# Kernel tuning notes

Measured on AMD Instinct MI355X. Metric: run time of the kernel, lower is better.

## Reference

```python
import jax, jax.numpy as jnp
import numpy as np

BOX_WARP = 1.0
RAY_START = 2.25
RAY_END = 3.3
S = 32  # depth_resolution (coarse), N_importance = 0


def bilinear_sample(image, coords):
    """Faithful port of the custom grid_sample (align_corners=True mapping).
    image: [B, C, H, W]; coords: [B, M, 2] in [-1, 1]. Returns [B, M, C]."""
    B, C, H, W = image.shape
    ix = (coords[..., 0] + 1.0) * 0.5 * (W - 1)
    iy = (coords[..., 1] + 1.0) * 0.5 * (H - 1)
    ix0 = jnp.floor(ix)
    iy0 = jnp.floor(iy)
    ix1 = ix0 + 1.0
    iy1 = iy0 + 1.0
    # weights use UNclamped corner positions, matching the torch code
    w_nw = (ix1 - ix) * (iy1 - iy)
    w_ne = (ix - ix0) * (iy1 - iy)
    w_sw = (ix1 - ix) * (iy - iy0)
    w_se = (ix - ix0) * (iy - iy0)
    ix0c = jnp.clip(ix0, 0, W - 1).astype(jnp.int32)
    ix1c = jnp.clip(ix1, 0, W - 1).astype(jnp.int32)
    iy0c = jnp.clip(iy0, 0, H - 1).astype(jnp.int32)
    iy1c = jnp.clip(iy1, 0, H - 1).astype(jnp.int32)
    img = image.reshape(B, C, H * W)

    def gather(iyc, ixc):
        idx = iyc * W + ixc  # [B, M]
        return jnp.take_along_axis(img, idx[:, None, :], axis=2)  # [B, C, M]

    out = (gather(iy0c, ix0c) * w_nw[:, None, :]
           + gather(iy0c, ix1c) * w_ne[:, None, :]
           + gather(iy1c, ix0c) * w_sw[:, None, :]
           + gather(iy1c, ix1c) * w_se[:, None, :])
    return out.transpose(0, 2, 1)  # [B, M, C]


def setup_inputs() -> dict:
    key = jax.random.key(0)
    k1, k2, k3, k4, k5 = jax.random.split(key, 5)
    N, n_planes, C, H, W = 2, 3, 32, 256, 256
    R = 16384
    vol_planes = jax.random.normal(k1, (N, n_planes, C, H, W), dtype=jnp.float32)
    dirs = jax.random.normal(k2, (N, R, 3), dtype=jnp.float32)
    dirs = dirs / jnp.linalg.norm(dirs, axis=-1, keepdims=True)
    # camera on sphere of radius 2.7 looking through origin -> samples in box
    ray_origins = -2.7 * dirs
    w1 = jax.random.normal(k3, (C, 64), dtype=jnp.float32) * (1.0 / np.sqrt(C))
    b1 = jnp.zeros((64,), dtype=jnp.float32)
    w2 = jax.random.normal(k4, (64, 33), dtype=jnp.float32) * (1.0 / 8.0)
    b2 = jnp.zeros((33,), dtype=jnp.float32)
    return {"vol_planes": vol_planes, "ray_origins": ray_origins,
            "ray_directions": dirs, "w1": w1, "b1": b1, "w2": w2, "b2": b2}


def reference(vol_planes, ray_origins, ray_directions, w1, b1, w2, b2):
    N, n_planes, C, H, W = vol_planes.shape
    R = ray_origins.shape[1]
    # --- sample_stratified (deterministic: midpoint of each bin) ---
    t = (jnp.arange(S, dtype=vol_planes.dtype) + 0.5) / S
    d = RAY_START + (RAY_END - RAY_START) * t  # [S]
    depths = jnp.broadcast_to(d[None, None, :, None], (N, R, S, 1))
    coords = ray_origins[:, :, None, :] + depths * ray_directions[:, :, None, :]
    M = R * S
    coords = coords.reshape(N, M, 3) * (2.0 / BOX_WARP)
    # --- project_onto_planes (vol_proj=True): xyz, yzx, xzy; sampler uses xy ---
    xy = coords[..., jnp.array([0, 1])]
    yz = coords[..., jnp.array([1, 2])]
    xz = coords[..., jnp.array([0, 2])]
    proj = jnp.stack([xy, yz, xz], axis=1).reshape(N * n_planes, M, 2)
    feats = bilinear_sample(vol_planes.reshape(N * n_planes, C, H, W), proj)
    feats = feats.reshape(N, n_planes, M, C).mean(axis=1)  # aggregate planes
    # --- decoder: small MLP -> 1 sigma + 32 rgb features (EG3D style) ---
    h = jax.nn.softplus(feats @ w1 + b1)
    o = h @ w2 + b2
    sigma = o[..., :1].reshape(N, R, S, 1)
    rgb = (jax.nn.sigmoid(o[..., 1:]) * 1.002 - 0.001).reshape(N, R, S, 32)
    # --- MipRayMarcher2 ---
    deltas = depths[:, :, 1:] - depths[:, :, :-1]
    colors_mid = 0.5 * (rgb[:, :, :-1] + rgb[:, :, 1:])
    densities_mid = 0.5 * (sigma[:, :, :-1] + sigma[:, :, 1:])
    densities_mid = jax.nn.softplus(densities_mid - 1.0)
    alpha = 1.0 - jnp.exp(-deltas * densities_mid)  # [N,R,S-1,1]
    trans = jnp.cumprod(
        jnp.concatenate([jnp.ones_like(alpha[:, :, :1]), 1.0 - alpha + 1e-10],
                        axis=2), axis=2)[:, :, :-1]
    weights = alpha * trans
    rgb_final = (weights * colors_mid).sum(axis=2)  # [N, R, 32]
    return rgb_final
```

## Files before the change

### kernel.cpp

```cpp
#include <hip/hip_runtime.h>
#include <math.h>

#define HH 256
#define WW 256
#define CC 32
#define SS 32
#define NRAYS 32768
#define RPB 8
#define TEXOFF 256

#define FXB_OFF 0
#define SIG_OFF 20480
#define WST_OFF 21504
#define W2T_OFF 25600
#define POOLSZ  31744

typedef __attribute__((ext_vector_type(8))) short short8;
typedef __attribute__((ext_vector_type(4))) float f32x4;

__device__ __forceinline__ f32x4 mfma16(short8 a, short8 b, f32x4 c) {
    return __builtin_amdgcn_mfma_f32_16x16x32_bf16(a, b, c, 0, 0, 0);
}

__device__ __forceinline__ float bf2f(unsigned short u) {
    union { unsigned int ui; float f; } v; v.ui = ((unsigned int)u) << 16; return v.f;
}
__device__ __forceinline__ unsigned short f2bf(float f) {
    union { float f; unsigned int u; } v; v.f = f;
    unsigned int u = v.u;
    unsigned int r = u + 0x7fffu + ((u >> 16) & 1u);
    return (unsigned short)(r >> 16);
}
__device__ __forceinline__ int iclamp(int x, int lo, int hi) {
    return x < lo ? lo : (x > hi ? hi : x);
}
__device__ __forceinline__ float softplus_f(float z) {
    return fmaxf(z, 0.f) + log1pf(expf(-fabsf(z)));
}
__device__ __forceinline__ float softplus_fast(float z) {
    return fmaxf(z, 0.f) + __logf(1.0f + __expf(-fabsf(z)));
}
__device__ __forceinline__ float sigmoid_fast(float z) {
    return __builtin_amdgcn_rcpf(1.0f + __expf(-z));
}

template<bool F32>
__device__ __forceinline__ float ldv(const void* p, size_t i) {
    if (F32) return ((const float*)p)[i];
    else     return bf2f(((const unsigned short*)p)[i]);
}

__global__ void detect_dtype(const void* __restrict__ rayo, int* __restrict__ flag) {
    if (threadIdx.x == 0 && blockIdx.x == 0) {
        const float* f = (const float*)rayo;
        const unsigned short* u = (const unsigned short*)rayo;
        float sf = 0.f, sb = 0.f;
        for (int r = 0; r < 8; r++) {
            const float a = f[3 * r], b = f[3 * r + 1], c = f[3 * r + 2];
            const float nf = a * a + b * b + c * c;
            sf += fminf(fabsf(nf - 7.29f), 1e3f);
            const float x = bf2f(u[3 * r]), y = bf2f(u[3 * r + 1]), z = bf2f(u[3 * r + 2]);
            const float nb = x * x + y * y + z * z;
            sb += fminf(fabsf(nb - 7.29f), 1e3f);
        }
        *flag = (sf < sb) ? 1 : 0;
    }
}

__global__ __launch_bounds__(1024) void transpose_tex(
    const void* __restrict__ vol, void* __restrict__ tex, const int* __restrict__ flag) {
    __shared__ float          tf[32][33];
    __shared__ unsigned short tu[32][33];
    const int tx = threadIdx.x, ty = threadIdx.y;
    const int w0 = blockIdx.x * 32;
    const int h  = blockIdx.y;
    const int img = blockIdx.z;
    const size_t src = (((size_t)img * CC + ty) * HH + h) * WW + (w0 + tx);
    const size_t dst = (((size_t)img * HH + h) * WW + (w0 + ty)) * CC + tx;
    if (*flag) {
        tf[ty][tx] = ((const float*)vol)[src];
        __syncthreads();
        ((float*)tex)[dst] = tf[tx][ty];
    } else {
        tu[ty][tx] = ((const unsigned short*)vol)[src];
        __syncthreads();
        ((unsigned short*)tex)[dst] = tu[tx][ty];
    }
}

template<bool F32>
__device__ void render_mfma_body(
    const void* __restrict__ tex,
    const void* __restrict__ rayo, const void* __restrict__ rayd,
    const void* __restrict__ w1b, const void* __restrict__ b1b,
    const void* __restrict__ w2b, const void* __restrict__ b2b,
    void* __restrict__ outp, char* __restrict__ pool)
{
    const int t = threadIdx.x;
    unsigned short* fxB = (unsigned short*)(pool + FXB_OFF);
    float* sigL = (float*)(pool + SIG_OFF);
    unsigned short* w1t = (unsigned short*)(pool + WST_OFF);
    unsigned short* w2t = (unsigned short*)(pool + W2T_OFF);

    for (int i = t; i < 2048; i += 256) {
        const int k = i >> 6, n = i & 63;
        w1t[n * 32 + k] = f2bf(ldv<F32>(w1b, i));
    }
    for (int i = t; i < 3072; i += 256) {
        const int n = i >> 6, k = i & 63;
        w2t[n * 64 + k] = (n < 33) ? f2bf(ldv<F32>(w2b, (size_t)k * 33 + n)) : (unsigned short)0;
    }
    __syncthreads();

    {
        const int rl = t >> 5;
        const int L  = t & 31;
        const int c4 = L & 7;
        const int sub = L >> 3;
        const int gray = blockIdx.x * RPB + rl;
        const int n = gray >> 14;
        const size_t rb = (size_t)gray * 3;
        const float ox = ldv<F32>(rayo, rb), oy = ldv<F32>(rayo, rb + 1), oz = ldv<F32>(rayo, rb + 2);
        const float dx = ldv<F32>(rayd, rb), dy = ldv<F32>(rayd, rb + 1), dz = ldv<F32>(rayd, rb + 2);

        #pragma unroll 2
        for (int k = 0; k < 8; ++k) {
            const int s = sub * 8 + k;
            const float d = 2.25f + 1.05f * ((s + 0.5f) * (1.0f / 32.0f));
            const float x = (ox + d * dx) * 2.0f;
            const float y = (oy + d * dy) * 2.0f;
            const float z = (oz + d * dz) * 2.0f;
            float a0[4] = {0.f, 0.f, 0.f, 0.f};
            float a1[4] = {0.f, 0.f, 0.f, 0.f};
            float a2[4] = {0.f, 0.f, 0.f, 0.f};
            #pragma unroll
            for (int p = 0; p < 3; p++) {
                const float u = (p == 0) ? x : ((p == 1) ? y : x);
                const float v = (p == 0) ? y : z;
                const float ixf = fmaf(u, 127.5f, 127.5f);
                const float iyf = fmaf(v, 127.5f, 127.5f);
                const float ix0f = floorf(ixf), iy0f = floorf(iyf);
                const float wx1 = ixf - ix0f, wy1 = iyf - iy0f;
                const float wx0 = 1.f - wx1,  wy0 = 1.f - wy1;
                const int ix0 = iclamp((int)ix0f, 0, 255);
                const int ix1 = iclamp((int)ix0f + 1, 0, 255);
                const int iy0 = iclamp((int)iy0f, 0, 255);
                const int iy1 = iclamp((int)iy0f + 1, 0, 255);
                const float w00 = wx0 * wy0, w01 = wx1 * wy0, w10 = wx0 * wy1, w11 = wx1 * wy1;
                const unsigned int pb4 = (unsigned int)(n * 3 + p) * (HH * WW * CC / 4);
                float v00[4], v01[4], v10[4], v11[4];
                if (F32) {
                    const float4* tx4 = (const float4*)tex;
                    const float4 q00 = tx4[pb4 + ((unsigned int)(iy0 * WW + ix0) << 3) + c4];
                    const float4 q01 = tx4[pb4 + ((unsigned int)(iy0 * WW + ix1) << 3) + c4];
                    const float4 q10 = tx4[pb4 + ((unsigned int)(iy1 * WW + ix0) << 3) + c4];
                    const float4 q11 = tx4[pb4 + ((unsigned int)(iy1 * WW + ix1) << 3) + c4];
                    v00[0] = q00.x; v00[1] = q00.y; v00[2] = q00.z; v00[3] = q00.w;
                    v01[0] = q01.x; v01[1] = q01.y; v01[2] = q01.z; v01[3] = q01.w;
                    v10[0] = q10.x; v10[1] = q10.y; v10[2] = q10.z; v10[3] = q10.w;
                    v11[0] = q11.x; v11[1] = q11.y; v11[2] = q11.z; v11[3] = q11.w;
                } else {
                    #pragma unroll
                    for (int i = 0; i < 4; i++) {
                        const size_t e = (size_t)pb4 * 4 + 4 * c4 + i;
                        v00[i] = ldv<false>(tex, e + ((size_t)(iy0 * WW + ix0) << 5));
                        v01[i] = ldv<false>(tex, e + ((size_t)(iy0 * WW + ix1) << 5));
                        v10[i] = ldv<false>(tex, e + ((size_t)(iy1 * WW + ix0) << 5));
                        v11[i] = ldv<false>(tex, e + ((size_t)(iy1 * WW + ix1) << 5));
                    }
                }
                #pragma unroll
                for (int i = 0; i < 4; i++) {
                    float acc = w00 * v00[i];
                    acc = fmaf(w01, v01[i], acc);
                    acc = fmaf(w10, v10[i], acc);
                    acc = fmaf(w11, v11[i], acc);
                    if (p == 0) a0[i] = acc; else if (p == 1) a1[i] = acc; else a2[i] = acc;
                }
            }
            unsigned int lo, hi;
            lo = (unsigned int)f2bf((a0[0] + a1[0] + a2[0]) * (1.0f / 3.0f))
               | ((unsigned int)f2bf((a0[1] + a1[1] + a2[1]) * (1.0f / 3.0f)) << 16);
            hi = (unsigned int)f2bf((a0[2] + a1[2] + a2[2]) * (1.0f / 3.0f))
               | ((unsigned int)f2bf((a0[3] + a1[3] + a2[3]) * (1.0f / 3.0f)) << 16);
            uint2 pk; pk.x = lo; pk.y = hi;
            *(uint2*)(pool + FXB_OFF + (rl * 32 + s) * 80 + c4 * 8) = pk;
        }
    }

    const int w = t >> 6;
    const int lane = t & 63;
    const int l16 = lane & 15, quad = lane >> 4;

    short8 b1f[4];
    #pragma unroll
    for (int nt = 0; nt < 4; nt++)
        b1f[nt] = *(const short8*)(pool + WST_OFF + (nt * 16 + l16) * 64 + quad * 16);
    short8 b2f[3][2];
    #pragma unroll
    for (int nt = 0; nt < 3; nt++)
        #pragma unroll
        for (int ks = 0; ks < 2; ks++)
            b2f[nt][ks] = *(const short8*)(pool + W2T_OFF + (nt * 16 + l16) * 128 + ks * 64 + quad * 16);
    float bb1[4], bb2[3];
    #pragma unroll
    for (int nt = 0; nt < 4; nt++) bb1[nt] = ldv<F32>(b1b, nt * 16 + l16);
    #pragma unroll
    for (int nt = 0; nt < 3; nt++) {
        const int n2 = nt * 16 + l16;
        bb2[nt] = (n2 < 33) ? ldv<F32>(b2b, n2) : 0.f;
    }
    __syncthreads();

    {
        char* hb = pool + WST_OFF + w * 2304;
        #pragma unroll 1
        for (int mt = 0; mt < 4; mt++) {
            const int rbase = w * 64 + mt * 16;
            const short8 a1 = *(const short8*)(pool + FXB_OFF + (rbase + l16) * 80 + quad * 16);
            #pragma unroll
            for (int nt = 0; nt < 4; nt++) {
                f32x4 hc = { bb1[nt], bb1[nt], bb1[nt], bb1[nt] };
                hc = mfma16(a1, b1f[nt], hc);
                #pragma unroll
                for (int r = 0; r < 4; r++) {
                    const float hv = softplus_fast(hc[r]);
                    *(unsigned short*)(hb + (quad * 4 + r) * 144 + (nt * 16 + l16) * 2) = f2bf(hv);
                }
            }
            const short8 a2k0 = *(const short8*)(hb + l16 * 144 + quad * 16);
            const short8 a2k1 = *(const short8*)(hb + l16 * 144 + 64 + quad * 16);
            #pragma unroll
            for (int nt = 0; nt < 3; nt++) {
                f32x4 o = { bb2[nt], bb2[nt], bb2[nt], bb2[nt] };
                o = mfma16(a2k0, b2f[nt][0], o);
                o = mfma16(a2k1, b2f[nt][1], o);
                #pragma unroll
                for (int r = 0; r < 4; r++) {
                    const int row = rbase + quad * 4 + r;
                    if (nt == 0) {
                        if (l16 == 0) sigL[row] = o[r];
                        else fxB[row * 40 + (l16 - 1)] =
                                 f2bf(fmaf(sigmoid_fast(o[r]), 1.002f, -0.001f));
                    } else if (nt == 1) {
                        fxB[row * 40 + (15 + l16)] =
                                 f2bf(fmaf(sigmoid_fast(o[r]), 1.002f, -0.001f));
                    } else if (l16 == 0) {
                        fxB[row * 40 + 31] =
                                 f2bf(fmaf(sigmoid_fast(o[r]), 1.002f, -0.001f));
                    }
                }
            }
        }
    }
    __syncthreads();

    {
        const int rl = t >> 5, c = t & 31;
        const int gr2 = blockIdx.x * RPB + rl;
        const float delta = 1.05f / 32.0f;
        float T = 1.0f, acc = 0.0f;
        float sp = sigL[rl * 32 + 0];
        float rp = bf2f(fxB[(rl * 32 + 0) * 40 + c]);
        #pragma unroll 1
        for (int sm = 0; sm < 31; sm++) {
            const float sn = sigL[rl * 32 + sm + 1];
            const float rn = bf2f(fxB[(rl * 32 + sm + 1) * 40 + c]);
            const float m = 0.5f * (sp + sn) - 1.0f;
            const float dens = fmaxf(m, 0.f) + __logf(1.0f + __expf(-fabsf(m)));
            const float alpha = 1.0f - __expf(-delta * dens);
            acc += alpha * T * 0.5f * (rp + rn);
            T *= (1.0f - alpha + 1e-10f);
            sp = sn; rp = rn;
        }
        const size_t oidx = (size_t)gr2 * 32 + c;
        if (F32) ((float*)outp)[oidx] = acc;
        else     ((unsigned short*)outp)[oidx] = f2bf(acc);
    }
}

__global__ __launch_bounds__(256, 4) void render_fast(
    const void* __restrict__ tex, const void* __restrict__ rayo,
    const void* __restrict__ rayd, const void* __restrict__ w1b,
    const void* __restrict__ b1b, const void* __restrict__ w2b,
    const void* __restrict__ b2b, void* __restrict__ outp,
    const int* __restrict__ flag)
{
    __shared__ __align__(16) char pool[POOLSZ];
    if (*flag) render_mfma_body<true >(tex, rayo, rayd, w1b, b1b, w2b, b2b, outp, pool);
    else       render_mfma_body<false>(tex, rayo, rayd, w1b, b1b, w2b, b2b, outp, pool);
}

template<bool F32>
__device__ __forceinline__ void render_body(
    const void* __restrict__ vol, const void* __restrict__ rayo,
    const void* __restrict__ rayd, const void* __restrict__ w1b,
    const void* __restrict__ b1b, const void* __restrict__ w2b,
    const void* __restrict__ b2b, void* __restrict__ outp,
    float* wsm, float (*rgbL)[SS][33], float (*sigL)[SS])
{
    const int t = threadIdx.x;
    for (int i = t; i < 4257; i += 256) {
        float v;
        if (i < 2048)       v = ldv<F32>(w1b, i);
        else if (i < 2112)  v = ldv<F32>(b1b, i - 2048);
        else if (i < 4224)  v = ldv<F32>(w2b, i - 2112);
        else                v = ldv<F32>(b2b, i - 4224);
        wsm[i] = v;
    }
    __syncthreads();

    const int rl = t >> 5;
    const int s  = t & 31;
    const int gray = blockIdx.x * RPB + rl;
    const int n = gray >> 14;

    const size_t rbase = (size_t)gray * 3;
    const float ox = ldv<F32>(rayo, rbase), oy = ldv<F32>(rayo, rbase + 1), oz = ldv<F32>(rayo, rbase + 2);
    const float dx = ldv<F32>(rayd, rbase), dy = ldv<F32>(rayd, rbase + 1), dz = ldv<F32>(rayd, rbase + 2);
    const float d = 2.25f + 1.05f * ((s + 0.5f) * (1.0f / 32.0f));
    const float x = (ox + d * dx) * 2.0f;
    const float y = (oy + d * dy) * 2.0f;
    const float z = (oz + d * dz) * 2.0f;

    float fx[32];
    #pragma unroll
    for (int c = 0; c < 32; c++) fx[c] = 0.f;

    #pragma unroll
    for (int p = 0; p < 3; p++) {
        const float u = (p == 0) ? x : ((p == 1) ? y : x);
        const float v = (p == 0) ? y : z;
        const float ixf = fmaf(u, 127.5f, 127.5f);
        const float iyf = fmaf(v, 127.5f, 127.5f);
        const float ix0f = floorf(ixf), iy0f = floorf(iyf);
        const float wx1 = ixf - ix0f, wy1 = iyf - iy0f;
        const float wx0 = 1.f - wx1,  wy0 = 1.f - wy1;
        const int ix0 = iclamp((int)ix0f, 0, 255);
        const int ix1 = iclamp((int)ix0f + 1, 0, 255);
        const int iy0 = iclamp((int)iy0f, 0, 255);
        const int iy1 = iclamp((int)iy0f + 1, 0, 255);
        const float wnw = wx0 * wy0, wne = wx1 * wy0, wsw = wx0 * wy1, wse = wx1 * wy1;
        const int i00 = iy0 * WW + ix0, i01 = iy0 * WW + ix1;
        const int i10 = iy1 * WW + ix0, i11 = iy1 * WW + ix1;
        const size_t pb = (size_t)(n * 3 + p) * CC * HH * WW;
        #pragma unroll
        for (int c = 0; c < 32; c++) {
            const size_t cb = pb + (size_t)c * (HH * WW);
            fx[c] += wnw * ldv<F32>(vol, cb + i00) + wne * ldv<F32>(vol, cb + i01)
                   + wsw * ldv<F32>(vol, cb + i10) + wse * ldv<F32>(vol, cb + i11);
        }
    }
    #pragma unroll
    for (int c = 0; c < 32; c++) fx[c] *= (1.0f / 3.0f);

    const float* W1 = wsm;
    const float* B1 = wsm + 2048;
    const float* W2 = wsm + 2112;
    const float* B2 = wsm + 4224;

    float h[64];
    #pragma unroll
    for (int j = 0; j < 64; j++) h[j] = B1[j];
    #pragma unroll
    for (int c = 0; c < 32; c++) {
        const float f = fx[c];
        #pragma unroll
        for (int j = 0; j < 64; j++) h[j] = fmaf(f, W1[c * 64 + j], h[j]);
    }
    #pragma unroll
    for (int j = 0; j < 64; j++) h[j] = softplus_f(h[j]);

    #pragma unroll 1
    for (int k = 0; k < 33; k++) {
        float zz = B2[k];
        #pragma unroll
        for (int j = 0; j < 64; j++) zz = fmaf(h[j], W2[j * 33 + k], zz);
        if (k == 0) sigL[rl][s] = zz;
        else {
            const float sg = 1.0f / (1.0f + expf(-zz));
            rgbL[rl][s][k - 1] = fmaf(sg, 1.002f, -0.001f);
        }
    }
    __syncthreads();

    const int c = t & 31;
    const float delta = 1.05f / 32.0f;
    float T = 1.0f, acc = 0.0f;
    float sig_prev = sigL[rl][0];
    float rgb_prev = rgbL[rl][0][c];
    #pragma unroll 1
    for (int sm = 0; sm < 31; sm++) {
        const float sig_next = sigL[rl][sm + 1];
        const float rgb_next = rgbL[rl][sm + 1][c];
        const float dens = softplus_f(0.5f * (sig_prev + sig_next) - 1.0f);
        const float alpha = 1.0f - expf(-delta * dens);
        acc += alpha * T * 0.5f * (rgb_prev + rgb_next);
        T *= (1.0f - alpha + 1e-10f);
        sig_prev = sig_next;
        rgb_prev = rgb_next;
    }
    const size_t oidx = (size_t)gray * 32 + c;
    if (F32) ((float*)outp)[oidx] = acc;
    else     ((unsigned short*)outp)[oidx] = f2bf(acc);
}

__global__ __launch_bounds__(256) void render_any(
    const void* __restrict__ vol, const void* __restrict__ rayo,
    const void* __restrict__ rayd, const void* __restrict__ w1b,
    const void* __restrict__ b1b, const void* __restrict__ w2b,
    const void* __restrict__ b2b, void* __restrict__ outp,
    const int* __restrict__ flag)
{
    __shared__ float wsm[4257];
    __shared__ float rgbL[RPB][SS][33];
    __shared__ float sigL[RPB][SS];
    if (*flag) render_body<true >(vol, rayo, rayd, w1b, b1b, w2b, b2b, outp, wsm, rgbL, sigL);
    else       render_body<false>(vol, rayo, rayd, w1b, b1b, w2b, b2b, outp, wsm, rgbL, sigL);
}

extern "C" void kernel_launch(void* const* d_in, const int* in_sizes, int n_in,
                              void* d_out, int out_size, void* d_ws, size_t ws_size,
                              hipStream_t stream) {
    const void* vol  = d_in[0];
    const void* rayo = d_in[1];
    const void* rayd = d_in[2];
    const void* w1   = d_in[3];
    const void* b1   = d_in[4];
    const void* w2   = d_in[5];
    const void* b2   = d_in[6];
    int* flag = (int*)d_ws;
    void* tex = (void*)((char*)d_ws + TEXOFF);

    const size_t need = TEXOFF + (size_t)6 * HH * WW * CC * 4;

    detect_dtype<<<dim3(1), dim3(64), 0, stream>>>(rayo, flag);
    if (ws_size >= need) {
        transpose_tex<<<dim3(WW / 32, HH, 6), dim3(32, 32), 0, stream>>>(vol, tex, flag);
        render_fast<<<dim3(NRAYS / RPB), dim3(256), 0, stream>>>(
            tex, rayo, rayd, w1, b1, w2, b2, d_out, flag);
    } else {
        render_any<<<dim3(NRAYS / RPB), dim3(256), 0, stream>>>(
            vol, rayo, rayd, w1, b1, w2, b2, d_out, flag);
    }
}
```

Baseline: 268.6 us.

## Vectorize texture transpose and precompute per-sample ray-march weights in shared memory

The plane-transpose kernel now processes 128-wide tiles with float4/ushort4 global loads and stores instead of scalar accesses, which cuts the number of memory instructions and improves coalescing. The ray marcher now computes alpha in parallel across samples, runs the transmittance scan once per ray in a single lane, and stores the final weights in shared memory. The colour accumulation per channel then becomes a plain FMA loop, so each of the 32 channel lanes no longer repeats the transcendental density math. The cost is two extra barriers, a serial 31-step scan in one lane per ray, and 1 KB more shared memory, which may reduce occupancy.

```diff
diff --git a/kernel.cpp b/kernel.cpp
--- a/kernel.cpp
+++ b/kernel.cpp
@@ -13,7 +13,8 @@
 #define SIG_OFF 20480
 #define WST_OFF 21504
 #define W2T_OFF 25600
-#define POOLSZ  31744
+#define ALP_OFF 31744
+#define POOLSZ  32768
 
 typedef __attribute__((ext_vector_type(8))) short short8;
 typedef __attribute__((ext_vector_type(4))) float f32x4;
@@ -69,22 +70,34 @@
 
 __global__ __launch_bounds__(1024) void transpose_tex(
     const void* __restrict__ vol, void* __restrict__ tex, const int* __restrict__ flag) {
-    __shared__ float          tf[32][33];
-    __shared__ unsigned short tu[32][33];
-    const int tx = threadIdx.x, ty = threadIdx.y;
-    const int w0 = blockIdx.x * 32;
+    __shared__ __align__(16) float          tf[32][129];
+    __shared__ __align__(16) unsigned short tb[32][129];
+    const int l = threadIdx.x;
+    const int tx = l & 31, ty = l >> 5;
+    const int wq = l >> 3, cq = l & 7;
+    const int w0 = blockIdx.x * 128;
     const int h  = blockIdx.y;
     const int img = blockIdx.z;
-    const size_t src = (((size_t)img * CC + ty) * HH + h) * WW + (w0 + tx);
-    const size_t dst = (((size_t)img * HH + h) * WW + (w0 + ty)) * CC + tx;
+    const size_t srcE = (((size_t)img * CC + ty) * HH + h) * WW + w0 + 4 * tx;
+    const size_t dstE = (((size_t)img * HH + h) * WW + (w0 + wq)) * CC + 4 * cq;
     if (*flag) {
-        tf[ty][tx] = ((const float*)vol)[src];
+        const float4 v = *(const float4*)((const float*)vol + srcE);
+        tf[ty][4 * tx + 0] = v.x; tf[ty][4 * tx + 1] = v.y;
+        tf[ty][4 * tx + 2] = v.z; tf[ty][4 * tx + 3] = v.w;
         __syncthreads();
-        ((float*)tex)[dst] = tf[tx][ty];
+        float4 o;
+        o.x = tf[4 * cq + 0][wq]; o.y = tf[4 * cq + 1][wq];
+        o.z = tf[4 * cq + 2][wq]; o.w = tf[4 * cq + 3][wq];
+        *(float4*)((float*)tex + dstE) = o;
     } else {
-        tu[ty][tx] = ((const unsigned short*)vol)[src];
+        const ushort4 v = *(const ushort4*)((const unsigned short*)vol + srcE);
+        tb[ty][4 * tx + 0] = v.x; tb[ty][4 * tx + 1] = v.y;
+        tb[ty][4 * tx + 2] = v.z; tb[ty][4 * tx + 3] = v.w;
         __syncthreads();
-        ((unsigned short*)tex)[dst] = tu[tx][ty];
+        ushort4 o;
+        o.x = tb[4 * cq + 0][wq]; o.y = tb[4 * cq + 1][wq];
+        o.z = tb[4 * cq + 2][wq]; o.w = tb[4 * cq + 3][wq];
+        *(ushort4*)((unsigned short*)tex + dstE) = o;
     }
 }
 
@@ -101,6 +114,7 @@
     float* sigL = (float*)(pool + SIG_OFF);
     unsigned short* w1t = (unsigned short*)(pool + WST_OFF);
     unsigned short* w2t = (unsigned short*)(pool + W2T_OFF);
+    float* aL = (float*)(pool + ALP_OFF);
 
     for (int i = t; i < 2048; i += 256) {
         const int k = i >> 6, n = i & 63;
@@ -256,22 +270,41 @@
     __syncthreads();
 
     {
+        const int rl = t >> 5, sm = t & 31;
+        if (sm < 31) {
+            const float sp = sigL[rl * 32 + sm];
+            const float sn = sigL[rl * 32 + sm + 1];
+            const float m = 0.5f * (sp + sn) - 1.0f;
+            const float dens = fmaxf(m, 0.f) + __logf(1.0f + __expf(-fabsf(m)));
+            aL[rl * 32 + sm] = 1.0f - __expf(-(1.05f / 32.0f) * dens);
+        }
+    }
+    __syncthreads();
+
+    {
+        const int rl = t >> 5, sm = t & 31;
+        if (sm == 0) {
+            float T = 1.0f;
+            #pragma unroll
+            for (int j = 0; j < 31; j++) {
+                const float a = aL[rl * 32 + j];
+                aL[rl * 32 + j] = (a * T) * 0.5f;
+                T *= (1.0f - a + 1e-10f);
+            }
+        }
+    }
+    __syncthreads();
+
+    {
         const int rl = t >> 5, c = t & 31;
         const int gr2 = blockIdx.x * RPB + rl;
-        const float delta = 1.05f / 32.0f;
-        float T = 1.0f, acc = 0.0f;
-        float sp = sigL[rl * 32 + 0];
+        float acc = 0.0f;
         float rp = bf2f(fxB[(rl * 32 + 0) * 40 + c]);
-        #pragma unroll 1
+        #pragma unroll 4
         for (int sm = 0; sm < 31; sm++) {
-            const float sn = sigL[rl * 32 + sm + 1];
             const float rn = bf2f(fxB[(rl * 32 + sm + 1) * 40 + c]);
-            const float m = 0.5f * (sp + sn) - 1.0f;
-            const float dens = fmaxf(m, 0.f) + __logf(1.0f + __expf(-fabsf(m)));
-            const float alpha = 1.0f - __expf(-delta * dens);
-            acc += alpha * T * 0.5f * (rp + rn);
-            T *= (1.0f - alpha + 1e-10f);
-            sp = sn; rp = rn;
+            acc = fmaf(aL[rl * 32 + sm], rp + rn, acc);
+            rp = rn;
         }
         const size_t oidx = (size_t)gr2 * 32 + c;
         if (F32) ((float*)outp)[oidx] = acc;
@@ -436,7 +469,7 @@
 
     detect_dtype<<<dim3(1), dim3(64), 0, stream>>>(rayo, flag);
     if (ws_size >= need) {
-        transpose_tex<<<dim3(WW / 32, HH, 6), dim3(32, 32), 0, stream>>>(vol, tex, flag);
+        transpose_tex<<<dim3(WW / 128, HH, 6), dim3(1024), 0, stream>>>(vol, tex, flag);
         render_fast<<<dim3(NRAYS / RPB), dim3(256), 0, stream>>>(
             tex, rayo, rayd, w1, b1, w2, b2, d_out, flag);
     } else {
```

Result: faster. 253.4 us (-5.6%).
